# Kernel optimization log

Hardware: AMD Instinct MI355X
Metric: run time of the kernel (lower is better)

Reference implementation:

```python
import jax, jax.numpy as jnp
import numpy as np

N_SKILLS = 1000
N_PROBLEMS = 20000
EMB = 256
TIME_LOG = 5.0
B, S = 32, 2048


def setup_inputs() -> dict:
    key = jax.random.key(0)
    ks = jax.random.split(key, 10)
    skills = jax.random.randint(ks[0], (B, S), 0, N_SKILLS, dtype=jnp.int64) if jax.config.jax_enable_x64 else jax.random.randint(ks[0], (B, S), 0, N_SKILLS, dtype=jnp.int32)
    problems = jax.random.randint(ks[1], (B, S), 0, N_PROBLEMS, dtype=skills.dtype)
    times = jnp.sort(jax.random.randint(ks[2], (B, S), 0, 10_000_000, dtype=skills.dtype), axis=-1)
    labels = jax.random.randint(ks[3], (B, S), 0, 2, dtype=skills.dtype)
    std = 0.01
    alpha_inter_W = std * jax.random.normal(ks[4], (2 * N_SKILLS, EMB), dtype=jnp.float32)
    alpha_skill_W = std * jax.random.normal(ks[5], (N_SKILLS, EMB), dtype=jnp.float32)
    beta_inter_W = std * jax.random.normal(ks[6], (2 * N_SKILLS, EMB), dtype=jnp.float32)
    beta_skill_W = std * jax.random.normal(ks[7], (N_SKILLS, EMB), dtype=jnp.float32)
    problem_base_W = std * jax.random.normal(ks[8], (N_PROBLEMS, 1), dtype=jnp.float32)
    skill_base_W = std * jax.random.normal(ks[9], (N_SKILLS, 1), dtype=jnp.float32)
    return {
        "skills": skills, "problems": problems, "times": times, "labels": labels,
        "alpha_inter_W": alpha_inter_W, "alpha_skill_W": alpha_skill_W,
        "beta_inter_W": beta_inter_W, "beta_skill_W": beta_skill_W,
        "problem_base_W": problem_base_W, "skill_base_W": skill_base_W,
    }


def reference(skills, problems, times, labels,
              alpha_inter_W, alpha_skill_W, beta_inter_W, beta_skill_W,
              problem_base_W, skill_base_W):
    n_skills = alpha_skill_W.shape[0]
    inters = skills + labels * n_skills  # [B,S]

    alpha_src = alpha_inter_W[inters]      # [B,S,E]
    alpha_tgt = alpha_skill_W[skills]      # [B,S,E]
    alphas = jnp.einsum("bse,bte->bst", alpha_src, alpha_tgt)  # [B,S,S]

    beta_src = beta_inter_W[inters]
    beta_tgt = beta_skill_W[skills]
    betas = jnp.einsum("bse,bte->bst", beta_src, beta_tgt)
    betas = jnp.clip(betas + 1.0, 0.0, 10.0)

    t = times.astype(jnp.float32) / 1000.0
    delta_t = jnp.abs(t[:, :, None] - t[:, None, :])
    delta_t = jnp.log(delta_t + 1e-10) / jnp.log(jnp.float32(TIME_LOG))

    cross = alphas * jnp.exp(-betas * delta_t)  # [B,S,S]

    seq_len = skills.shape[1]
    # original keeps strict upper triangle (source i strictly before target j)
    keep = jnp.triu(jnp.ones((seq_len, seq_len), dtype=cross.dtype), k=1)
    sum_t = jnp.sum(cross * keep[None], axis=-2)  # sum over source dim -> [B,S]

    problem_bias = problem_base_W[problems][..., 0]  # [B,S]
    skill_bias = skill_base_W[skills][..., 0]        # [B,S]
    h = problem_bias + skill_bias + sum_t
    return jax.nn.sigmoid(h)
```

## Files before the change

kernel.cpp:

```cpp
#include <hip/hip_runtime.h>
#include <hip/hip_bf16.h>
#include <stdint.h>

#define NSK   1000
#define EMB   256
#define BB    32
#define SS    2048
#define TI    128
#define TJ    64
#define NUNITB 272
#define BK    64
#define NCHUNK (EMB / BK)
#define LDSB  24576
#define SCALE_INV (1.0f / 4096.0f)

typedef float f32x16 __attribute__((ext_vector_type(16)));
typedef float f32x4  __attribute__((ext_vector_type(4)));
typedef long  longx2 __attribute__((ext_vector_type(2)));

#define OFF_AI8 0
#define OFF_BI8 (2 * NSK * EMB)
#define OFF_AS8 (4 * NSK * EMB)
#define OFF_BS8 (5 * NSK * EMB)
#define TOT8    (6 * NSK * EMB)

__global__ void cvt_tables(const float* __restrict__ ai, const float* __restrict__ bi,
                           const float* __restrict__ as_, const float* __restrict__ bs,
                           int* __restrict__ ws8, float* __restrict__ acc) {
    int g = blockIdx.x * 256 + threadIdx.x;
    if (g < BB * SS) acc[g] = 0.0f;
    if (g * 4 >= TOT8) return;
    int e = g * 4;
    const float* src; int off;
    if (e < OFF_AS8) { if (e < OFF_BI8) { src = ai;  off = e; }
                       else             { src = bi;  off = e - OFF_BI8; } }
    else             { if (e < OFF_BS8) { src = as_; off = e - OFF_AS8; }
                       else             { src = bs;  off = e - OFF_BS8; } }
    const float4 v = *(const float4*)(src + off);
    int lo = __builtin_amdgcn_cvt_pk_fp8_f32(v.x * 64.0f, v.y * 64.0f, 0, false);
    int wd = __builtin_amdgcn_cvt_pk_fp8_f32(v.z * 64.0f, v.w * 64.0f, lo, true);
    ws8[g] = wd;
}

__device__ __attribute__((noinline)) float dot256(const float* __restrict__ a,
                                                  const float* __restrict__ b) {
    float s = 0.0f;
#pragma unroll 8
    for (int k = 0; k < EMB; ++k) s += a[k] * b[k];
    return s;
}

__global__ __launch_bounds__(256, 2) void hawkes_unit(
    const int* __restrict__ skills, const int* __restrict__ times,
    const int* __restrict__ labels, const unsigned char* __restrict__ tab,
    const float* __restrict__ aiW_f, const float* __restrict__ asW_f,
    const float* __restrict__ biW_f, const float* __restrict__ bsW_f,
    float* __restrict__ acc)
{
    __shared__ __align__(16) char  sbuf[2 * LDSB];
    __shared__ __align__(16) float t_i[TI];
    __shared__ __align__(16) float t_j[TJ];
    __shared__ int   idx_i[TI];
    __shared__ int   idx_j[TJ];
    __shared__ float colsum[TJ];

    const int u  = blockIdx.x;
    const int b  = u / NUNITB;
    const int p  = u - b * NUNITB;
    int m = (int)sqrtf((float)p);
    while ((m + 1) * (m + 2) <= p) ++m;
    while (m * (m + 1) > p) --m;
    int jt, it;
    if (p >= (m + 1) * (m + 1)) { jt = 2 * m + 1; it = p - (m + 1) * (m + 1); }
    else                        { jt = 2 * m;     it = p - m * (m + 1); }
    const int j0 = jt * TJ, i0 = it * TI;
    const bool partial = (i0 + TI - 1 >= j0);

    const int tid = threadIdx.x;
    const int l   = tid & 63;
    const int w   = tid >> 6;
    const int wi  = w >> 1, wj = w & 1;
    const int lane31 = l & 31;
    const int khalf  = l >> 5;

    if (tid < TJ) {
        int j = j0 + tid;
        idx_j[tid] = skills[b * SS + j];
        t_j[tid]   = (float)times[b * SS + j] / 1000.0f;
        colsum[tid] = 0.0f;
    } else if (tid < TJ + TI) {
        int q = tid - TJ;
        int ii = i0 + q;
        idx_i[q] = skills[b * SS + ii] + labels[b * SS + ii] * NSK;
        t_i[q]   = (float)times[b * SS + ii] / 1000.0f;
    }
    __syncthreads();

    const float tjv = t_j[wj * 32 + lane31];
    const int   jl  = wj * 32 + lane31;

    const unsigned char* rowptr[3];
    int wo[3];
#pragma unroll
    for (int s = 0; s < 3; ++s) {
        int mm = w * 3 + s;
        int tabbase, ldsbase, row;
        if (mm < 8) {
            int mb = mm & 3;
            tabbase = (mm < 4) ? OFF_AI8 : OFF_BI8;
            ldsbase = ((mm < 4) ? 0 : 8192) + mb * 2048;
            row = idx_i[mb * 32 + (l >> 1)];
        } else {
            int mb = mm & 1;
            tabbase = (mm < 10) ? OFF_AS8 : OFF_BS8;
            ldsbase = ((mm < 10) ? 16384 : 20480) + mb * 2048;
            row = idx_j[mb * 32 + (l >> 1)];
        }
        rowptr[s] = tab + tabbase + (size_t)row * EMB + (l & 1) * 32;
        wo[s] = ldsbase + (l & 1) * 1024 + (l >> 1) * 8;
    }

#define LOADC(dst, c)                                                  \
    do { _Pragma("unroll")                                             \
        for (int s = 0; s < 3; ++s) {                                  \
            dst[s][0] = *(const longx2*)(rowptr[s] + (c) * BK);        \
            dst[s][1] = *(const longx2*)(rowptr[s] + (c) * BK + 16);   \
        }                                                              \
    } while (0)
#define WRITEC(src, buf)                                               \
    do { char* db = sbuf + (buf) * LDSB;                               \
        _Pragma("unroll")                                              \
        for (int s = 0; s < 3; ++s) {                                  \
            *(long*)(db + wo[s])             = src[s][0].x;            \
            *(long*)(db + wo[s] + 256)       = src[s][0].y;            \
            *(long*)(db + wo[s] + 512)       = src[s][1].x;            \
            *(long*)(db + wo[s] + 512 + 256) = src[s][1].y;            \
        }                                                              \
    } while (0)

    f32x16 accA[2], accB[2];
#pragma unroll
    for (int mi = 0; mi < 2; ++mi) { accA[mi] = 0.0f; accB[mi] = 0.0f; }

    longx2 sreg[3][2];
    LOADC(sreg, 0);
    WRITEC(sreg, 0);

    for (int c = 0; c < NCHUNK; ++c) {
        if (c + 1 < NCHUNK) LOADC(sreg, c + 1);
        __syncthreads();

        const char* sb = sbuf + (c & 1) * LDSB;
#pragma unroll
        for (int ks = 0; ks < 4; ++ks) {
            long fa[2], fb[2], ga, gb;
#pragma unroll
            for (int mi = 0; mi < 2; ++mi) {
                int mb = (wi * 2 + mi) * 2048 + ks * 512 + l * 8;
                fa[mi] = *(const long*)(sb + 0    + mb);
                fb[mi] = *(const long*)(sb + 8192 + mb);
            }
            {
                int nb = wj * 2048 + ks * 512 + l * 8;
                ga = *(const long*)(sb + 16384 + nb);
                gb = *(const long*)(sb + 20480 + nb);
            }
#pragma unroll
            for (int mi = 0; mi < 2; ++mi) {
                accA[mi] = __builtin_amdgcn_mfma_f32_32x32x16_fp8_fp8(
                    fa[mi], ga, accA[mi], 0, 0, 0);
                accB[mi] = __builtin_amdgcn_mfma_f32_32x32x16_fp8_fp8(
                    fb[mi], gb, accB[mi], 0, 0, 0);
            }
        }

        if (c + 1 < NCHUNK) WRITEC(sreg, (c + 1) & 1);
    }

    float csum = 0.0f;
#pragma unroll
    for (int mi = 0; mi < 2; ++mi) {
        const int rbase = (wi * 2 + mi) * 32 + 4 * khalf;
        f32x4 tiv[4];
#pragma unroll
        for (int q = 0; q < 4; ++q) tiv[q] = *(const f32x4*)(t_i + rbase + 8 * q);
#pragma unroll
        for (int r = 0; r < 16; ++r) {
            const int q = r >> 2, e = r & 3;
            const int il = rbase + 8 * q + e;
            if (partial && i0 + il >= j0 + jl) continue;
            float d = fabsf(tiv[q][e] - tjv);
            float alpha, braw;
            if (d == 0.0f) {
                alpha = dot256(aiW_f + (size_t)idx_i[il] * EMB,
                               asW_f + (size_t)idx_j[jl] * EMB) * 4096.0f;
                braw  = dot256(biW_f + (size_t)idx_i[il] * EMB,
                               bsW_f + (size_t)idx_j[jl] * EMB) * 4096.0f;
            } else {
                alpha = accA[mi][r];
                braw  = accB[mi][r];
            }
            float dl   = __builtin_amdgcn_logf(d + 1e-10f) * 0.6213349345596119f;
            float beta = braw * SCALE_INV + 1.0f;
            csum += alpha * __builtin_amdgcn_exp2f(-beta * dl);
        }
    }
    csum *= SCALE_INV;

    __syncthreads();
    csum += __shfl_xor(csum, 32);
    if (l < 32)
        atomicAdd(&colsum[wj * 32 + lane31], csum);
    __syncthreads();
    if (tid < TJ)
        atomicAdd(&acc[b * SS + j0 + tid], colsum[tid]);
}

__global__ void hawkes_final(const int* __restrict__ skills, const int* __restrict__ problems,
                             const float* __restrict__ pbW, const float* __restrict__ sbW,
                             float* __restrict__ out) {
    int i = blockIdx.x * 256 + threadIdx.x;
    if (i >= BB * SS) return;
    float h = pbW[problems[i]] + sbW[skills[i]] + out[i];
    out[i] = 1.0f / (1.0f + __builtin_amdgcn_exp2f(-h * 1.4426950408889634f));
}

extern "C" void kernel_launch(void* const* d_in, const int* in_sizes, int n_in,
                              void* d_out, int out_size, void* d_ws, size_t ws_size,
                              hipStream_t stream) {
    const int*   skills   = (const int*)d_in[0];
    const int*   problems = (const int*)d_in[1];
    const int*   times    = (const int*)d_in[2];
    const int*   labels   = (const int*)d_in[3];
    const float* aiW      = (const float*)d_in[4];
    const float* asW      = (const float*)d_in[5];
    const float* biW      = (const float*)d_in[6];
    const float* bsW      = (const float*)d_in[7];
    const float* pbW      = (const float*)d_in[8];
    const float* sbW      = (const float*)d_in[9];
    float* out = (float*)d_out;
    unsigned char* tab = (unsigned char*)d_ws;

    cvt_tables<<<(TOT8 / 4 + 255) / 256, 256, 0, stream>>>(aiW, biW, asW, bsW,
                                                           (int*)tab, out);
    hawkes_unit<<<BB * NUNITB, 256, 0, stream>>>(skills, times, labels, tab,
                                                 aiW, asW, biW, bsW, out);
    hawkes_final<<<(BB * SS + 255) / 256, 256, 0, stream>>>(skills, problems, pbW, sbW, out);
}
```

Baseline: 178.3 us.

## Load B-operand fragments directly from global into registers, shrink LDS, raise occupancy

The j-side skill embeddings (B operand of the FP8 MFMAs) are now gathered by each lane straight from global memory into registers instead of being staged through shared memory. This shrinks the double-buffered LDS tile from 24 KB to 16 KB per buffer and cuts the per-warp staging loads, and launch bounds rise to allow four blocks per SM. In exchange each warp issues its own uncoalesced 8-byte global reads, which may be duplicated across warps, and register pressure under the tighter launch bound may cause spills.

Measured after the change: 243.8 us. 1.37x slower.

```diff
diff --git a/kernel.cpp b/kernel.cpp
--- a/kernel.cpp
+++ b/kernel.cpp
@@ -11,7 +11,7 @@
 #define NUNITB 272
 #define BK    64
 #define NCHUNK (EMB / BK)
-#define LDSB  24576
+#define LDSB  16384
 #define SCALE_INV (1.0f / 4096.0f)
 
 typedef float f32x16 __attribute__((ext_vector_type(16)));
@@ -50,7 +50,7 @@
     return s;
 }
 
-__global__ __launch_bounds__(256, 2) void hawkes_unit(
+__global__ __launch_bounds__(256, 4) void hawkes_unit(
     const int* __restrict__ skills, const int* __restrict__ times,
     const int* __restrict__ labels, const unsigned char* __restrict__ tab,
     const float* __restrict__ aiW_f, const float* __restrict__ asW_f,
@@ -96,33 +96,28 @@
     }
     __syncthreads();
 
-    const float tjv = t_j[wj * 32 + lane31];
     const int   jl  = wj * 32 + lane31;
-
-    const unsigned char* rowptr[3];
-    int wo[3];
-#pragma unroll
-    for (int s = 0; s < 3; ++s) {
-        int mm = w * 3 + s;
-        int tabbase, ldsbase, row;
-        if (mm < 8) {
-            int mb = mm & 3;
-            tabbase = (mm < 4) ? OFF_AI8 : OFF_BI8;
-            ldsbase = ((mm < 4) ? 0 : 8192) + mb * 2048;
-            row = idx_i[mb * 32 + (l >> 1)];
-        } else {
-            int mb = mm & 1;
-            tabbase = (mm < 10) ? OFF_AS8 : OFF_BS8;
-            ldsbase = ((mm < 10) ? 16384 : 20480) + mb * 2048;
-            row = idx_j[mb * 32 + (l >> 1)];
-        }
+    const float tjv = t_j[jl];
+    const int   jskill = idx_j[jl];
+    const unsigned char* aspB = tab + OFF_AS8 + (size_t)jskill * EMB + khalf * 8;
+    const unsigned char* bspB = tab + OFF_BS8 + (size_t)jskill * EMB + khalf * 8;
+
+    const unsigned char* rowptr[2];
+    int wo[2];
+#pragma unroll
+    for (int s = 0; s < 2; ++s) {
+        int mm = w * 2 + s;
+        int mb = mm & 3;
+        int tabbase = (mm < 4) ? OFF_AI8 : OFF_BI8;
+        int ldsbase = ((mm < 4) ? 0 : 8192) + mb * 2048;
+        int row = idx_i[mb * 32 + (l >> 1)];
         rowptr[s] = tab + tabbase + (size_t)row * EMB + (l & 1) * 32;
         wo[s] = ldsbase + (l & 1) * 1024 + (l >> 1) * 8;
     }
 
 #define LOADC(dst, c)                                                  \
     do { _Pragma("unroll")                                             \
-        for (int s = 0; s < 3; ++s) {                                  \
+        for (int s = 0; s < 2; ++s) {                                  \
             dst[s][0] = *(const longx2*)(rowptr[s] + (c) * BK);        \
             dst[s][1] = *(const longx2*)(rowptr[s] + (c) * BK + 16);   \
         }                                                              \
@@ -130,20 +125,29 @@
 #define WRITEC(src, buf)                                               \
     do { char* db = sbuf + (buf) * LDSB;                               \
         _Pragma("unroll")                                              \
-        for (int s = 0; s < 3; ++s) {                                  \
+        for (int s = 0; s < 2; ++s) {                                  \
             *(long*)(db + wo[s])             = src[s][0].x;            \
             *(long*)(db + wo[s] + 256)       = src[s][0].y;            \
             *(long*)(db + wo[s] + 512)       = src[s][1].x;            \
             *(long*)(db + wo[s] + 512 + 256) = src[s][1].y;            \
         }                                                              \
     } while (0)
+#define GATHB(c)                                                       \
+    do { _Pragma("unroll")                                             \
+        for (int ks = 0; ks < 4; ++ks) {                               \
+            gra[ks] = *(const long*)(aspB + (c) * BK + ks * 16);       \
+            grb[ks] = *(const long*)(bspB + (c) * BK + ks * 16);       \
+        }                                                              \
+    } while (0)
 
     f32x16 accA[2], accB[2];
 #pragma unroll
     for (int mi = 0; mi < 2; ++mi) { accA[mi] = 0.0f; accB[mi] = 0.0f; }
 
-    longx2 sreg[3][2];
+    longx2 sreg[2][2];
+    long gra[4], grb[4];
     LOADC(sreg, 0);
+    GATHB(0);
     WRITEC(sreg, 0);
 
     for (int c = 0; c < NCHUNK; ++c) {
@@ -153,28 +157,23 @@
         const char* sb = sbuf + (c & 1) * LDSB;
 #pragma unroll
         for (int ks = 0; ks < 4; ++ks) {
-            long fa[2], fb[2], ga, gb;
+            long fa[2], fb[2];
 #pragma unroll
             for (int mi = 0; mi < 2; ++mi) {
-                int mb = (wi * 2 + mi) * 2048 + ks * 512 + l * 8;
-                fa[mi] = *(const long*)(sb + 0    + mb);
-                fb[mi] = *(const long*)(sb + 8192 + mb);
-            }
-            {
-                int nb = wj * 2048 + ks * 512 + l * 8;
-                ga = *(const long*)(sb + 16384 + nb);
-                gb = *(const long*)(sb + 20480 + nb);
+                int mb2 = (wi * 2 + mi) * 2048 + ks * 512 + l * 8;
+                fa[mi] = *(const long*)(sb + 0    + mb2);
+                fb[mi] = *(const long*)(sb + 8192 + mb2);
             }
 #pragma unroll
             for (int mi = 0; mi < 2; ++mi) {
                 accA[mi] = __builtin_amdgcn_mfma_f32_32x32x16_fp8_fp8(
-                    fa[mi], ga, accA[mi], 0, 0, 0);
+                    fa[mi], gra[ks], accA[mi], 0, 0, 0);
                 accB[mi] = __builtin_amdgcn_mfma_f32_32x32x16_fp8_fp8(
-                    fb[mi], gb, accB[mi], 0, 0, 0);
+                    fb[mi], grb[ks], accB[mi], 0, 0, 0);
             }
         }
 
-        if (c + 1 < NCHUNK) WRITEC(sreg, (c + 1) & 1);
+        if (c + 1 < NCHUNK) { GATHB(c + 1); WRITEC(sreg, (c + 1) & 1); }
     }
 
     float csum = 0.0f;
@@ -193,9 +192,9 @@
             float alpha, braw;
             if (d == 0.0f) {
                 alpha = dot256(aiW_f + (size_t)idx_i[il] * EMB,
-                               asW_f + (size_t)idx_j[jl] * EMB) * 4096.0f;
+                               asW_f + (size_t)jskill * EMB) * 4096.0f;
                 braw  = dot256(biW_f + (size_t)idx_i[il] * EMB,
-                               bsW_f + (size_t)idx_j[jl] * EMB) * 4096.0f;
+                               bsW_f + (size_t)jskill * EMB) * 4096.0f;
             } else {
                 alpha = accA[mi][r];
                 braw  = accB[mi][r];
```

## Swizzle LDS layout for 128-bit fragment loads and raise occupancy hint

Applied to the files above, without the earlier changes.

Reorganizes the shared-memory tile layout so each lane stores and loads 16-byte vectors with an XOR swizzle, replacing four 8-byte LDS reads per MFMA group with two 16-byte reads. The K-steps of each vector are fed to two MFMAs in sequence. This reduces LDS instruction count and bank conflicts in the inner loop. Launch bounds also move from 2 to 3 blocks per SM, which limits registers per thread and may cause spills.

Result: slower. 182.5 us (+2.4%).

```diff
diff --git a/kernel.cpp b/kernel.cpp
--- a/kernel.cpp
+++ b/kernel.cpp
@@ -50,7 +50,7 @@
     return s;
 }
 
-__global__ __launch_bounds__(256, 2) void hawkes_unit(
+__global__ __launch_bounds__(256, 3) void hawkes_unit(
     const int* __restrict__ skills, const int* __restrict__ times,
     const int* __restrict__ labels, const unsigned char* __restrict__ tab,
     const float* __restrict__ aiW_f, const float* __restrict__ asW_f,
@@ -99,8 +99,14 @@
     const float tjv = t_j[wj * 32 + lane31];
     const int   jl  = wj * 32 + lane31;
 
+    const int rsw = ((l >> 1) & 1) * 3;
+    const int rb0 = lane31 * 64 + 16 * ((2 * khalf + 0) ^ rsw);
+    const int rb1 = lane31 * 64 + 16 * ((2 * khalf + 1) ^ rsw);
+
     const unsigned char* rowptr[3];
-    int wo[3];
+    int wadr0[3], wadr1[3];
+    const int wr  = l >> 1, wa = l & 1;
+    const int wsw = ((wr >> 1) & 1) * 3;
 #pragma unroll
     for (int s = 0; s < 3; ++s) {
         int mm = w * 3 + s;
@@ -109,15 +115,16 @@
             int mb = mm & 3;
             tabbase = (mm < 4) ? OFF_AI8 : OFF_BI8;
             ldsbase = ((mm < 4) ? 0 : 8192) + mb * 2048;
-            row = idx_i[mb * 32 + (l >> 1)];
+            row = idx_i[mb * 32 + wr];
         } else {
             int mb = mm & 1;
             tabbase = (mm < 10) ? OFF_AS8 : OFF_BS8;
             ldsbase = ((mm < 10) ? 16384 : 20480) + mb * 2048;
-            row = idx_j[mb * 32 + (l >> 1)];
+            row = idx_j[mb * 32 + wr];
         }
-        rowptr[s] = tab + tabbase + (size_t)row * EMB + (l & 1) * 32;
-        wo[s] = ldsbase + (l & 1) * 1024 + (l >> 1) * 8;
+        rowptr[s] = tab + tabbase + (size_t)row * EMB + wa * 32;
+        wadr0[s] = ldsbase + wr * 64 + 16 * ((0 + wa) ^ wsw);
+        wadr1[s] = ldsbase + wr * 64 + 16 * ((2 + wa) ^ wsw);
     }
 
 #define LOADC(dst, c)                                                  \
@@ -131,10 +138,11 @@
     do { char* db = sbuf + (buf) * LDSB;                               \
         _Pragma("unroll")                                              \
         for (int s = 0; s < 3; ++s) {                                  \
-            *(long*)(db + wo[s])             = src[s][0].x;            \
-            *(long*)(db + wo[s] + 256)       = src[s][0].y;            \
-            *(long*)(db + wo[s] + 512)       = src[s][1].x;            \
-            *(long*)(db + wo[s] + 512 + 256) = src[s][1].y;            \
+            longx2 w0, w1;                                             \
+            w0.x = src[s][0].x; w0.y = src[s][1].x;                    \
+            w1.x = src[s][0].y; w1.y = src[s][1].y;                    \
+            *(longx2*)(db + wadr0[s]) = w0;                            \
+            *(longx2*)(db + wadr1[s]) = w1;                            \
         }                                                              \
     } while (0)
 
@@ -152,25 +160,30 @@
 
         const char* sb = sbuf + (c & 1) * LDSB;
 #pragma unroll
-        for (int ks = 0; ks < 4; ++ks) {
-            long fa[2], fb[2], ga, gb;
+        for (int h = 0; h < 2; ++h) {
+            const int ro = h ? rb1 : rb0;
+            longx2 FA[2], FB[2], GA, GB;
 #pragma unroll
             for (int mi = 0; mi < 2; ++mi) {
-                int mb = (wi * 2 + mi) * 2048 + ks * 512 + l * 8;
-                fa[mi] = *(const long*)(sb + 0    + mb);
-                fb[mi] = *(const long*)(sb + 8192 + mb);
-            }
-            {
-                int nb = wj * 2048 + ks * 512 + l * 8;
-                ga = *(const long*)(sb + 16384 + nb);
-                gb = *(const long*)(sb + 20480 + nb);
-            }
+                const int mb2 = (wi * 2 + mi) * 2048 + ro;
+                FA[mi] = *(const longx2*)(sb + 0    + mb2);
+                FB[mi] = *(const longx2*)(sb + 8192 + mb2);
+            }
+            GA = *(const longx2*)(sb + 16384 + wj * 2048 + ro);
+            GB = *(const longx2*)(sb + 20480 + wj * 2048 + ro);
 #pragma unroll
             for (int mi = 0; mi < 2; ++mi) {
                 accA[mi] = __builtin_amdgcn_mfma_f32_32x32x16_fp8_fp8(
-                    fa[mi], ga, accA[mi], 0, 0, 0);
+                    FA[mi].x, GA.x, accA[mi], 0, 0, 0);
                 accB[mi] = __builtin_amdgcn_mfma_f32_32x32x16_fp8_fp8(
-                    fb[mi], gb, accB[mi], 0, 0, 0);
+                    FB[mi].x, GB.x, accB[mi], 0, 0, 0);
+            }
+#pragma unroll
+            for (int mi = 0; mi < 2; ++mi) {
+                accA[mi] = __builtin_amdgcn_mfma_f32_32x32x16_fp8_fp8(
+                    FA[mi].y, GA.y, accA[mi], 0, 0, 0);
+                accB[mi] = __builtin_amdgcn_mfma_f32_32x32x16_fp8_fp8(
+                    FB[mi].y, GB.y, accB[mi], 0, 0, 0);
             }
         }
 
```

## Enlarge j-tile to 128 so each block computes a square 128x128 triangle tile

Applied to the files above, without the earlier changes.

Changes the column tile from 64 to 128, making tiles square and rewriting the triangular tile-index mapping to a simple triangular-number inverse. Each wave now computes a 2x2 grid of MFMA accumulators, reusing loaded A/B fragments across two column blocks and halving the number of blocks per batch. This cuts redundant gathering of row embeddings and per-block setup, at the cost of doubled accumulator registers (64 extra VGPRs of accumulators), larger LDS per block, and more wasted work on diagonal tiles.

Measured after the change: 192.4 us. 1.08x slower.

```diff
diff --git a/kernel.cpp b/kernel.cpp
--- a/kernel.cpp
+++ b/kernel.cpp
@@ -7,11 +7,11 @@
 #define BB    32
 #define SS    2048
 #define TI    128
-#define TJ    64
-#define NUNITB 272
+#define TJ    128
+#define NUNITB 136
 #define BK    64
 #define NCHUNK (EMB / BK)
-#define LDSB  24576
+#define LDSB  32768
 #define SCALE_INV (1.0f / 4096.0f)
 
 typedef float f32x16 __attribute__((ext_vector_type(16)));
@@ -67,12 +67,10 @@
     const int u  = blockIdx.x;
     const int b  = u / NUNITB;
     const int p  = u - b * NUNITB;
-    int m = (int)sqrtf((float)p);
-    while ((m + 1) * (m + 2) <= p) ++m;
-    while (m * (m + 1) > p) --m;
-    int jt, it;
-    if (p >= (m + 1) * (m + 1)) { jt = 2 * m + 1; it = p - (m + 1) * (m + 1); }
-    else                        { jt = 2 * m;     it = p - m * (m + 1); }
+    int jt = (int)((sqrtf(8.0f * (float)p + 1.0f) - 1.0f) * 0.5f);
+    while ((jt + 1) * (jt + 2) / 2 <= p) ++jt;
+    while (jt * (jt + 1) / 2 > p) --jt;
+    const int it = p - jt * (jt + 1) / 2;
     const int j0 = jt * TJ, i0 = it * TI;
     const bool partial = (i0 + TI - 1 >= j0);
 
@@ -88,7 +86,7 @@
         idx_j[tid] = skills[b * SS + j];
         t_j[tid]   = (float)times[b * SS + j] / 1000.0f;
         colsum[tid] = 0.0f;
-    } else if (tid < TJ + TI) {
+    } else {
         int q = tid - TJ;
         int ii = i0 + q;
         idx_i[q] = skills[b * SS + ii] + labels[b * SS + ii] * NSK;
@@ -96,24 +94,20 @@
     }
     __syncthreads();
 
-    const float tjv = t_j[wj * 32 + lane31];
-    const int   jl  = wj * 32 + lane31;
-
-    const unsigned char* rowptr[3];
-    int wo[3];
-#pragma unroll
-    for (int s = 0; s < 3; ++s) {
-        int mm = w * 3 + s;
+    const unsigned char* rowptr[4];
+    int wo[4];
+#pragma unroll
+    for (int s = 0; s < 4; ++s) {
+        int mm = w * 4 + s;
+        int mb = mm & 3;
         int tabbase, ldsbase, row;
         if (mm < 8) {
-            int mb = mm & 3;
             tabbase = (mm < 4) ? OFF_AI8 : OFF_BI8;
             ldsbase = ((mm < 4) ? 0 : 8192) + mb * 2048;
             row = idx_i[mb * 32 + (l >> 1)];
         } else {
-            int mb = mm & 1;
-            tabbase = (mm < 10) ? OFF_AS8 : OFF_BS8;
-            ldsbase = ((mm < 10) ? 16384 : 20480) + mb * 2048;
+            tabbase = (mm < 12) ? OFF_AS8 : OFF_BS8;
+            ldsbase = ((mm < 12) ? 16384 : 24576) + mb * 2048;
             row = idx_j[mb * 32 + (l >> 1)];
         }
         rowptr[s] = tab + tabbase + (size_t)row * EMB + (l & 1) * 32;
@@ -122,7 +116,7 @@
 
 #define LOADC(dst, c)                                                  \
     do { _Pragma("unroll")                                             \
-        for (int s = 0; s < 3; ++s) {                                  \
+        for (int s = 0; s < 4; ++s) {                                  \
             dst[s][0] = *(const longx2*)(rowptr[s] + (c) * BK);        \
             dst[s][1] = *(const longx2*)(rowptr[s] + (c) * BK + 16);   \
         }                                                              \
@@ -130,7 +124,7 @@
 #define WRITEC(src, buf)                                               \
     do { char* db = sbuf + (buf) * LDSB;                               \
         _Pragma("unroll")                                              \
-        for (int s = 0; s < 3; ++s) {                                  \
+        for (int s = 0; s < 4; ++s) {                                  \
             *(long*)(db + wo[s])             = src[s][0].x;            \
             *(long*)(db + wo[s] + 256)       = src[s][0].y;            \
             *(long*)(db + wo[s] + 512)       = src[s][1].x;            \
@@ -138,11 +132,13 @@
         }                                                              \
     } while (0)
 
-    f32x16 accA[2], accB[2];
-#pragma unroll
-    for (int mi = 0; mi < 2; ++mi) { accA[mi] = 0.0f; accB[mi] = 0.0f; }
-
-    longx2 sreg[3][2];
+    f32x16 accA[2][2], accB[2][2];
+#pragma unroll
+    for (int mi = 0; mi < 2; ++mi)
+#pragma unroll
+        for (int nj = 0; nj < 2; ++nj) { accA[mi][nj] = 0.0f; accB[mi][nj] = 0.0f; }
+
+    longx2 sreg[4][2];
     LOADC(sreg, 0);
     WRITEC(sreg, 0);
 
@@ -153,31 +149,37 @@
         const char* sb = sbuf + (c & 1) * LDSB;
 #pragma unroll
         for (int ks = 0; ks < 4; ++ks) {
-            long fa[2], fb[2], ga, gb;
+            long fa[2], fb[2], ga[2], gb[2];
 #pragma unroll
             for (int mi = 0; mi < 2; ++mi) {
-                int mb = (wi * 2 + mi) * 2048 + ks * 512 + l * 8;
-                fa[mi] = *(const long*)(sb + 0    + mb);
-                fb[mi] = *(const long*)(sb + 8192 + mb);
+                int mb2 = (wi * 2 + mi) * 2048 + ks * 512 + l * 8;
+                fa[mi] = *(const long*)(sb + 0    + mb2);
+                fb[mi] = *(const long*)(sb + 8192 + mb2);
             }
-            {
-                int nb = wj * 2048 + ks * 512 + l * 8;
-                ga = *(const long*)(sb + 16384 + nb);
-                gb = *(const long*)(sb + 20480 + nb);
+#pragma unroll
+            for (int nj = 0; nj < 2; ++nj) {
+                int nb2 = (wj * 2 + nj) * 2048 + ks * 512 + l * 8;
+                ga[nj] = *(const long*)(sb + 16384 + nb2);
+                gb[nj] = *(const long*)(sb + 24576 + nb2);
             }
 #pragma unroll
-            for (int mi = 0; mi < 2; ++mi) {
-                accA[mi] = __builtin_amdgcn_mfma_f32_32x32x16_fp8_fp8(
-                    fa[mi], ga, accA[mi], 0, 0, 0);
-                accB[mi] = __builtin_amdgcn_mfma_f32_32x32x16_fp8_fp8(
-                    fb[mi], gb, accB[mi], 0, 0, 0);
-            }
+            for (int mi = 0; mi < 2; ++mi)
+#pragma unroll
+                for (int nj = 0; nj < 2; ++nj) {
+                    accA[mi][nj] = __builtin_amdgcn_mfma_f32_32x32x16_fp8_fp8(
+                        fa[mi], ga[nj], accA[mi][nj], 0, 0, 0);
+                    accB[mi][nj] = __builtin_amdgcn_mfma_f32_32x32x16_fp8_fp8(
+                        fb[mi], gb[nj], accB[mi][nj], 0, 0, 0);
+                }
         }
 
         if (c + 1 < NCHUNK) WRITEC(sreg, (c + 1) & 1);
     }
 
-    float csum = 0.0f;
+    float csum[2] = {0.0f, 0.0f};
+    const int   jl0  = wj * 64 + lane31;
+    const float tjv[2] = { t_j[jl0], t_j[jl0 + 32] };
+    const int   jsk[2] = { idx_j[jl0], idx_j[jl0 + 32] };
 #pragma unroll
     for (int mi = 0; mi < 2; ++mi) {
         const int rbase = (wi * 2 + mi) * 32 + 4 * khalf;
@@ -188,29 +190,38 @@
         for (int r = 0; r < 16; ++r) {
             const int q = r >> 2, e = r & 3;
             const int il = rbase + 8 * q + e;
-            if (partial && i0 + il >= j0 + jl) continue;
-            float d = fabsf(tiv[q][e] - tjv);
-            float alpha, braw;
-            if (d == 0.0f) {
-                alpha = dot256(aiW_f + (size_t)idx_i[il] * EMB,
-                               asW_f + (size_t)idx_j[jl] * EMB) * 4096.0f;
-                braw  = dot256(biW_f + (size_t)idx_i[il] * EMB,
-                               bsW_f + (size_t)idx_j[jl] * EMB) * 4096.0f;
-            } else {
-                alpha = accA[mi][r];
-                braw  = accB[mi][r];
+            const float ti = tiv[q][e];
+#pragma unroll
+            for (int nj = 0; nj < 2; ++nj) {
+                const int jl = jl0 + nj * 32;
+                if (partial && i0 + il >= j0 + jl) continue;
+                float d = fabsf(ti - tjv[nj]);
+                float alpha, braw;
+                if (d == 0.0f) {
+                    alpha = dot256(aiW_f + (size_t)idx_i[il] * EMB,
+                                   asW_f + (size_t)jsk[nj] * EMB) * 4096.0f;
+                    braw  = dot256(biW_f + (size_t)idx_i[il] * EMB,
+                                   bsW_f + (size_t)jsk[nj] * EMB) * 4096.0f;
+                } else {
+                    alpha = accA[mi][nj][r];
+                    braw  = accB[mi][nj][r];
+                }
+                float dl   = __builtin_amdgcn_logf(d + 1e-10f) * 0.6213349345596119f;
+                float beta = braw * SCALE_INV + 1.0f;
+                csum[nj] += alpha * __builtin_amdgcn_exp2f(-beta * dl);
             }
-            float dl   = __builtin_amdgcn_logf(d + 1e-10f) * 0.6213349345596119f;
-            float beta = braw * SCALE_INV + 1.0f;
-            csum += alpha * __builtin_amdgcn_exp2f(-beta * dl);
         }
     }
-    csum *= SCALE_INV;
+    csum[0] *= SCALE_INV;
+    csum[1] *= SCALE_INV;
 
     __syncthreads();
-    csum += __shfl_xor(csum, 32);
-    if (l < 32)
-        atomicAdd(&colsum[wj * 32 + lane31], csum);
+#pragma unroll
+    for (int nj = 0; nj < 2; ++nj) {
+        float cs = csum[nj] + __shfl_xor(csum[nj], 32);
+        if (l < 32)
+            atomicAdd(&colsum[wj * 64 + nj * 32 + lane31], cs);
+    }
     __syncthreads();
     if (tid < TJ)
         atomicAdd(&acc[b * SS + j0 + tid], colsum[tid]);
```
